# Kernel tuning notes

Hardware: AMD Instinct MI355X
Metric: run time of the kernel (lower is better)

The kernel has to match this reference:

```python
import jax, jax.numpy as jnp
import numpy as np

EMBED_DIM = 1024
NUM_HEADS = 16
HEAD_DIM = EMBED_DIM // NUM_HEADS
ROPE_BASE = 10000.0


def rotate_half(x):
    d = x.shape[-1] // 2
    x1, x2 = x[..., :d], x[..., d:]
    return jnp.concatenate((-x2, x1), axis=-1)


def setup_inputs() -> dict:
    key = jax.random.key(0)
    k_x, k_wqkv, k_bqkv, k_wo, k_bo = jax.random.split(key, 5)
    C = EMBED_DIM
    x = jax.random.normal(k_x, (4, 2048, C), dtype=jnp.float32)
    s = 1.0 / np.sqrt(C)
    W_qkv = jax.random.uniform(k_wqkv, (C, 3 * C), minval=-s, maxval=s, dtype=jnp.float32)
    b_qkv = jax.random.uniform(k_bqkv, (3 * C,), minval=-s, maxval=s, dtype=jnp.float32)
    W_out = jax.random.uniform(k_wo, (C, C), minval=-s, maxval=s, dtype=jnp.float32)
    b_out = jax.random.uniform(k_bo, (C,), minval=-s, maxval=s, dtype=jnp.float32)
    return {"x": x, "W_qkv": W_qkv, "b_qkv": b_qkv, "W_out": W_out, "b_out": b_out}


def reference(x, W_qkv, b_qkv, W_out, b_out):
    B, T, C = x.shape
    H, Dh = NUM_HEADS, HEAD_DIM
    # fused QKV projection: [B,T,3C] -> [3,B,H,T,Dh]
    qkv = (x @ W_qkv + b_qkv).reshape(B, T, 3, H, Dh).transpose(2, 0, 3, 1, 4)
    q, k, v = qkv[0], qkv[1], qkv[2]
    # rotary embedding: freqs [T, Dh/2] -> emb [T, Dh]
    inv_freq = 1.0 / (ROPE_BASE ** (jnp.arange(0, Dh, 2, dtype=jnp.float32) / Dh))
    freqs = jnp.arange(T, dtype=jnp.float32)[:, None] * inv_freq[None, :]
    emb = jnp.concatenate((freqs, freqs), axis=-1)  # [T, Dh], broadcasts over B,H
    cos, sin = jnp.cos(emb), jnp.sin(emb)
    q = q * cos + rotate_half(q) * sin
    k = k * cos + rotate_half(k) * sin
    # full (non-causal) attention, manual softmax
    scale = 1.0 / np.sqrt(Dh)
    attn = jax.nn.softmax(jnp.einsum("bhqd,bhkd->bhqk", q, k) * scale, axis=-1)
    out = jnp.einsum("bhqk,bhkd->bhqd", attn, v)  # [B,H,T,Dh]
    out = out.transpose(0, 2, 1, 3).reshape(B, T, C)
    return out @ W_out + b_out
```

## Files before the change

### kernel.cpp

```cpp
#include <hip/hip_runtime.h>
#include <math.h>

#define T_SEQ 2048
#define CDIM  1024
#define NH    16
#define DHD   64
#define BATCH 4
#define MROWS (BATCH * T_SEQ)
#define BHN   (BATCH * NH)

typedef _Float16 f16;
typedef __attribute__((ext_vector_type(8))) _Float16 f16x8;
typedef __attribute__((ext_vector_type(4))) _Float16 f16x4;
typedef __attribute__((ext_vector_type(2))) _Float16 f16x2;
typedef __attribute__((ext_vector_type(2))) __fp16 fp16x2;
typedef __attribute__((ext_vector_type(4))) float f32x4;

__device__ __forceinline__ float fast_exp2(float x) {
#if __has_builtin(__builtin_amdgcn_exp2f)
    return __builtin_amdgcn_exp2f(x);
#else
    return exp2f(x);
#endif
}

__device__ __forceinline__ float fast_rcp(float x) {
#if __has_builtin(__builtin_amdgcn_rcpf)
    return __builtin_amdgcn_rcpf(x);
#else
    return 1.0f / x;
#endif
}

__device__ __forceinline__ f16x2 cvt_pk_f16(float a, float b) {
    fp16x2 r = __builtin_amdgcn_cvt_pkrtz(a, b);
    return __builtin_bit_cast(f16x2, r);
}

__device__ __forceinline__ void gl_lds16(const f16* g, f16* l) {
    __builtin_amdgcn_global_load_lds(
        (const __attribute__((address_space(1))) void*)(g),
        (__attribute__((address_space(3))) void*)(l),
        16, 0, 0);
}

__global__ __launch_bounds__(256) void prep_kernel(
    const float* __restrict__ X, f16* __restrict__ Xf,
    const float* __restrict__ Wq, const float* __restrict__ Wo,
    f16* __restrict__ Wqt, f16* __restrict__ Wot,
    float* __restrict__ ctab, float* __restrict__ stab)
{
    const int bx = blockIdx.x;
    if (bx < 256) {
        int idx = bx * 256 + threadIdx.x;
        int t = idx >> 5, i = idx & 31;
        double inv = pow(10000.0, -(double)(2 * i) / 64.0);
        double a = (double)t * inv;
        ctab[idx] = (float)cos(a);
        stab[idx] = (float)sin(a);
    } else if (bx < 4352) {
        int idx = (bx - 256) * 256 + threadIdx.x;
        const float4* src = (const float4*)X + (size_t)idx * 2;
        float4 a = src[0], b = src[1];
        f16x8 o;
        o[0] = (f16)a.x; o[1] = (f16)a.y; o[2] = (f16)a.z; o[3] = (f16)a.w;
        o[4] = (f16)b.x; o[5] = (f16)b.y; o[6] = (f16)b.z; o[7] = (f16)b.w;
        *((f16x8*)Xf + idx) = o;
    } else {
        const int sub = threadIdx.x >> 6, lane = threadIdx.x & 63;
        const int id = (bx - 4352) * 4 + sub;
        const int k0 = (id & 127) * 8;
        const int ny = id >> 7;
        const float* W;
        f16* Wt;
        int N, n;
        if (ny < 48) { W = Wq; Wt = Wqt; N = 3072; n = ny * 64 + lane; }
        else         { W = Wo; Wt = Wot; N = 1024; n = (ny - 48) * 64 + lane; }
        f16x8 o;
#pragma unroll
        for (int j = 0; j < 8; j++) o[j] = (f16)W[(size_t)(k0 + j) * N + n];
        *(f16x8*)(Wt + (size_t)n * CDIM + k0) = o;
    }
}

#define GEMM_MAINLOOP(Aimg, Bimg, M0, N0)                                         \
    __shared__ f16 As[128][64], Bs[128][64];                                      \
    const int tid = threadIdx.x, wave = tid >> 6, lane = tid & 63;                \
    const int l16 = lane & 15, quad = lane >> 4;                                  \
    const int wm = wave >> 1, wn = wave & 1;                                      \
    f32x4 acc[4][4];                                                              \
    _Pragma("unroll") for (int i = 0; i < 4; i++)                                 \
        _Pragma("unroll") for (int j = 0; j < 4; j++)                             \
            acc[i][j] = (f32x4){0.f, 0.f, 0.f, 0.f};                              \
    const f16* sbase = (wave < 2) ? (Aimg) : (Bimg);                              \
    f16* lbase = ((wave < 2) ? &As[0][0] : &Bs[0][0]) + (wave & 1) * 4096;        \
    const size_t srow0 = ((wave < 2) ? (size_t)(M0) : (size_t)(N0)) + (wave & 1) * 64; \
    const int srow = lane >> 3, schunk = lane & 7;                                \
    const int gchunk = (schunk ^ srow) << 3;         \
    for (int k0 = 0; k0 < CDIM; k0 += 64) {                                       \
        _Pragma("unroll") for (int it = 0; it < 8; it++)                          \
            gl_lds16(sbase + (srow0 + it * 8 + srow) * CDIM + k0 + gchunk,        \
                     lbase + it * 512);                                           \
        __syncthreads();                                                          \
        _Pragma("unroll") for (int ks = 0; ks < 2; ks++) {                        \
            f16x8 fa[4], fb[4];                                                   \
            _Pragma("unroll") for (int mi = 0; mi < 4; mi++)                      \
                fa[mi] = *(const f16x8*)                                          \
                    &As[wm * 64 + mi * 16 + l16][((ks * 4 + quad) ^ (l16 & 7)) << 3]; \
            _Pragma("unroll") for (int ni = 0; ni < 4; ni++)                      \
                fb[ni] = *(const f16x8*)                                          \
                    &Bs[wn * 64 + ni * 16 + l16][((ks * 4 + quad) ^ (l16 & 7)) << 3]; \
            _Pragma("unroll") for (int mi = 0; mi < 4; mi++)                      \
                _Pragma("unroll") for (int ni = 0; ni < 4; ni++)                  \
                    acc[mi][ni] = __builtin_amdgcn_mfma_f32_16x16x32_f16(         \
                        fa[mi], fb[ni], acc[mi][ni], 0, 0, 0);                    \
        }                                                                         \
        __syncthreads();                                                          \
    }

__global__ __launch_bounds__(256) void qkv_gemm_kernel(
    const f16* __restrict__ Xf, const f16* __restrict__ Wt,
    const float* __restrict__ bias,
    const float* __restrict__ ctab, const float* __restrict__ stab,
    f16* __restrict__ qf, f16* __restrict__ kf, f16* __restrict__ vtb)
{
    const int m0 = blockIdx.x * 128;
    const int n0 = blockIdx.y * 128;
    GEMM_MAINLOOP(Xf, Wt, m0, n0)

    const int ncol0 = n0 + wn * 64;
    const int w = ncol0 >> 10;
    const int h = (ncol0 >> 6) & 15;
    const int b = m0 >> 11;
    const int trow0 = (m0 & 2047) + wm * 64 + quad * 4;
    float bia[4];
#pragma unroll
    for (int ni = 0; ni < 4; ni++) bia[ni] = bias[ncol0 + ni * 16 + l16];

    if (w < 2) {
        f16* oq = w ? kf : qf;
        const float sc = w ? 1.0f : 0.18033688011112042f;
#pragma unroll
        for (int mi = 0; mi < 4; mi++) {
#pragma unroll
            for (int i = 0; i < 4; i++) {
                int t = trow0 + mi * 16 + i;
                size_t rowoff = ((size_t)(b * NH + h) * T_SEQ + t) * DHD;
#pragma unroll
                for (int np = 0; np < 2; np++) {
                    int d = np * 16 + l16;
                    float v0 = acc[mi][np][i] + bia[np];
                    float v1 = acc[mi][np + 2][i] + bia[np + 2];
                    float c = ctab[(t << 5) + d];
                    float s = stab[(t << 5) + d];
                    oq[rowoff + d]      = (f16)((v0 * c - v1 * s) * sc);
                    oq[rowoff + d + 32] = (f16)((v1 * c + v0 * s) * sc);
                }
            }
        }
    } else {
#pragma unroll
        for (int mi = 0; mi < 4; mi++) {
            const int tb = trow0 + mi * 16;
#pragma unroll
            for (int ni = 0; ni < 4; ni++) {
                const int d = ni * 16 + l16;
                f16x4 pv;
#pragma unroll
                for (int i = 0; i < 4; i++) pv[i] = (f16)(acc[mi][ni][i] + bia[ni]);
                *(f16x4*)(vtb + ((size_t)(b * NH + h) * DHD + d) * T_SEQ + tb) = pv;
            }
        }
    }
}

__global__ __launch_bounds__(256, 4) void attn_kernel(
    const f16* __restrict__ qf, const f16* __restrict__ kf,
    const f16* __restrict__ vt, f16* __restrict__ ab)
{
    __shared__ f16 Kb[2][64][64];
    __shared__ f16 Vb[2][64][64];

    const int tid  = threadIdx.x;
    const int wave = tid >> 6, lane = tid & 63;
    const int l16  = lane & 15, quad = lane >> 4;

    const int flat = blockIdx.x + (blockIdx.y << 4);
    const int swz  = (flat & 7) * 128 + (flat >> 3);
    const int qt = swz & 15;
    const int bh = swz >> 4;
    const int q0 = qt * 128 + wave * 32;

    const f16* kbase = kf + (size_t)bh * T_SEQ * DHD;
    const f16* vbase = vt + (size_t)bh * DHD * T_SEQ;

    f16x8 qfr[2][2];
#pragma unroll
    for (int qs = 0; qs < 2; qs++) {
        const f16* qrow = qf + ((size_t)bh * T_SEQ + q0 + qs * 16 + l16) * DHD;
        qfr[qs][0] = *(const f16x8*)(qrow + quad * 8);
        qfr[qs][1] = *(const f16x8*)(qrow + 32 + quad * 8);
    }

    f32x4 o[2][4];
    f32x4 lacc[2];
#pragma unroll
    for (int qs = 0; qs < 2; qs++) {
        lacc[qs] = (f32x4){0.f, 0.f, 0.f, 0.f};
#pragma unroll
        for (int dt = 0; dt < 4; dt++) o[qs][dt] = (f32x4){0.f, 0.f, 0.f, 0.f};
    }
    f16x4 ones4;
#pragma unroll
    for (int j = 0; j < 4; j++) ones4[j] = (f16)1.0f;

    const int srow = tid >> 3;
    const int schunk = tid & 7;
    const int gcol = (schunk ^ (srow & 7)) << 3;

#define STAGE(t, b)                                                               \
    {                                                                             \
        const f16* kg = kbase + ((size_t)(t) * 64 + srow) * DHD + gcol;           \
        const f16* vg = vbase + (size_t)srow * T_SEQ + (t) * 64 + gcol;           \
        f16* kl = &Kb[b][wave * 8][0];                                            \
        f16* vl = &Vb[b][wave * 8][0];                                            \
        gl_lds16(kg, kl);                                                         \
        gl_lds16(kg + 32 * DHD, kl + 32 * 64);                                    \
        gl_lds16(vg, vl);                                                         \
        gl_lds16(vg + (size_t)32 * T_SEQ, vl + 32 * 64);                          \
    }

    STAGE(0, 0)
    __syncthreads();

    for (int kt = 0; kt < 32; kt++) {
        const int buf = kt & 1;
        if (kt < 31) STAGE(kt + 1, buf ^ 1)

#pragma unroll
        for (int half = 0; half < 2; half++) {
            f32x4 sc[2][2];
#pragma unroll
            for (int k2 = 0; k2 < 2; k2++)
#pragma unroll
                for (int qs = 0; qs < 2; qs++) sc[k2][qs] = (f32x4){0.f, 0.f, 0.f, 0.f};
            __builtin_amdgcn_s_setprio(1);
#pragma unroll
            for (int k2 = 0; k2 < 2; k2++) {
                const int keyt = half * 2 + k2;
#pragma unroll
                for (int ks = 0; ks < 2; ks++) {
                    const int kc = ((ks * 4 + quad) ^ (l16 & 7)) << 3;
                    f16x8 kfr = *(const f16x8*)&Kb[buf][keyt * 16 + l16][kc];
#pragma unroll
                    for (int qs = 0; qs < 2; qs++)
                        sc[k2][qs] = __builtin_amdgcn_mfma_f32_16x16x32_f16(
                            kfr, qfr[qs][ks], sc[k2][qs], 0, 0, 0);
                }
            }
            __builtin_amdgcn_s_setprio(0);
            f16x4 pp[2][2];
#pragma unroll
            for (int k2 = 0; k2 < 2; k2++) {
#pragma unroll
                for (int qs = 0; qs < 2; qs++) {
                    ((f16x2*)&pp[k2][qs])[0] = cvt_pk_f16(
                        fast_exp2(sc[k2][qs][0]), fast_exp2(sc[k2][qs][1]));
                    ((f16x2*)&pp[k2][qs])[1] = cvt_pk_f16(
                        fast_exp2(sc[k2][qs][2]), fast_exp2(sc[k2][qs][3]));
                }
            }
            __builtin_amdgcn_s_setprio(1);
#pragma unroll
            for (int qs = 0; qs < 2; qs++)
#pragma unroll
                for (int k2 = 0; k2 < 2; k2++)
                    lacc[qs] = __builtin_amdgcn_mfma_f32_16x16x16f16(
                        pp[k2][qs], ones4, lacc[qs], 0, 0, 0);
#pragma unroll
            for (int dt = 0; dt < 4; dt++) {
#pragma unroll
                for (int c = 0; c < 2; c++) {
                    const int vc = ((half * 4 + c * 2 + (quad >> 1)) ^ (l16 & 7)) * 8
                                 + (quad & 1) * 4;
                    f16x4 vfr = *(const f16x4*)&Vb[buf][dt * 16 + l16][vc];
#pragma unroll
                    for (int qs = 0; qs < 2; qs++)
                        o[qs][dt] = __builtin_amdgcn_mfma_f32_16x16x16f16(
                            pp[c][qs], vfr, o[qs][dt], 0, 0, 0);
                }
            }
            __builtin_amdgcn_s_setprio(0);
        }

        if (kt < 31) __syncthreads();
    }
#undef STAGE

    const int b = bh >> 4, h = bh & 15;
#pragma unroll
    for (int qs = 0; qs < 2; qs++) {
#pragma unroll
        for (int i = 0; i < 4; i++) {
            float iv = fast_rcp(lacc[qs][i]);
            int m = b * T_SEQ + qt * 128 + wave * 32 + qs * 16 + quad * 4 + i;
#pragma unroll
            for (int dt = 0; dt < 4; dt++)
                ab[(size_t)m * CDIM + h * 64 + dt * 16 + l16] = (f16)(o[qs][dt][i] * iv);
        }
    }
}

__global__ __launch_bounds__(256) void out_gemm_kernel(
    const f16* __restrict__ Ab, const f16* __restrict__ Wt,
    const float* __restrict__ bias, float* __restrict__ out)
{
    const int m0 = blockIdx.x * 128;
    const int n0 = blockIdx.y * 128;
    GEMM_MAINLOOP(Ab, Wt, m0, n0)

    const int ncol0 = n0 + wn * 64;
    float bia[4];
#pragma unroll
    for (int ni = 0; ni < 4; ni++) bia[ni] = bias[ncol0 + ni * 16 + l16];
#pragma unroll
    for (int mi = 0; mi < 4; mi++) {
#pragma unroll
        for (int i = 0; i < 4; i++) {
            int m = m0 + wm * 64 + mi * 16 + quad * 4 + i;
#pragma unroll
            for (int ni = 0; ni < 4; ni++)
                out[(size_t)m * CDIM + ncol0 + ni * 16 + l16] = acc[mi][ni][i] + bia[ni];
        }
    }
}

extern "C" void kernel_launch(void* const* d_in, const int* in_sizes, int n_in,
                              void* d_out, int out_size, void* d_ws, size_t ws_size,
                              hipStream_t stream)
{
    const float* x    = (const float*)d_in[0];
    const float* Wqkv = (const float*)d_in[1];
    const float* bqkv = (const float*)d_in[2];
    const float* Wout = (const float*)d_in[3];
    const float* bout = (const float*)d_in[4];
    float* out = (float*)d_out;

    const size_t XSZ  = (size_t)MROWS * CDIM;
    const size_t WQSZ = (size_t)3072 * CDIM;
    const size_t WOSZ = (size_t)CDIM * CDIM;
    const size_t QSZ  = (size_t)BHN * T_SEQ * DHD;

    char* p = (char*)d_ws;
    f16* Xf  = (f16*)p; p += XSZ * 2;
    f16* Wqt = (f16*)p; p += WQSZ * 2;
    f16* Wot = (f16*)p; p += WOSZ * 2;
    f16* qf  = (f16*)p; p += QSZ * 2;
    f16* kf  = (f16*)p; p += QSZ * 2;
    f16* vtb = (f16*)p; p += QSZ * 2;
    f16* ab  = (f16*)p; p += QSZ * 2;
    float* ctab = (float*)p; p += T_SEQ * 32 * 4;
    float* stab = (float*)p; p += T_SEQ * 32 * 4;

    prep_kernel<<<6400, 256, 0, stream>>>(x, Xf, Wqkv, Wout, Wqt, Wot, ctab, stab);
    qkv_gemm_kernel<<<dim3(64, 24), 256, 0, stream>>>(
        Xf, Wqt, bqkv, ctab, stab, qf, kf, vtb);
    attn_kernel<<<dim3(16, BHN), 256, 0, stream>>>(qf, kf, vtb, ab);
    out_gemm_kernel<<<dim3(64, 8), 256, 0, stream>>>(ab, Wot, bout, out);
}
```

Baseline: 276.4 us.

## Switch attention to 32x32x16 MFMA tiles with permlane-swapped P operands

Rewrites the attention inner loop to use 32x32x16 f16 MFMAs for both QK^T and PV instead of 16x16 tiles. The exp'd probabilities are repacked into the A-operand layout with v_permlane32_swap, so no LDS round trip is needed. The row sum is now accumulated on the VALU and reduced through a cross-half shuffle plus a small LDS buffer, replacing the ones-vector MFMA. The aim is fewer MFMA issues and fewer LDS reads per tile, at the cost of larger accumulator register pressure and an extra barrier at the end.

```diff
diff --git a/kernel.cpp b/kernel.cpp
--- a/kernel.cpp
+++ b/kernel.cpp
@@ -15,6 +15,8 @@
 typedef __attribute__((ext_vector_type(2))) _Float16 f16x2;
 typedef __attribute__((ext_vector_type(2))) __fp16 fp16x2;
 typedef __attribute__((ext_vector_type(4))) float f32x4;
+typedef __attribute__((ext_vector_type(16))) float f32x16;
+typedef __attribute__((ext_vector_type(4))) unsigned int uint4v;
 
 __device__ __forceinline__ float fast_exp2(float x) {
 #if __has_builtin(__builtin_amdgcn_exp2f)
@@ -35,6 +37,10 @@
 __device__ __forceinline__ f16x2 cvt_pk_f16(float a, float b) {
     fp16x2 r = __builtin_amdgcn_cvt_pkrtz(a, b);
     return __builtin_bit_cast(f16x2, r);
+}
+
+__device__ __forceinline__ void permlane32_swap(unsigned &a, unsigned &b) {
+    asm volatile("v_permlane32_swap_b32 %0, %1" : "+v"(a), "+v"(b));
 }
 
 __device__ __forceinline__ void gl_lds16(const f16* g, f16* l) {
@@ -180,10 +186,11 @@
 {
     __shared__ f16 Kb[2][64][64];
     __shared__ f16 Vb[2][64][64];
+    __shared__ float Lb[4][32];
 
     const int tid  = threadIdx.x;
     const int wave = tid >> 6, lane = tid & 63;
-    const int l16  = lane & 15, quad = lane >> 4;
+    const int l31  = lane & 31, hh = lane >> 5;
 
     const int flat = blockIdx.x + (blockIdx.y << 4);
     const int swz  = (flat & 7) * 128 + (flat >> 3);
@@ -194,25 +201,20 @@
     const f16* kbase = kf + (size_t)bh * T_SEQ * DHD;
     const f16* vbase = vt + (size_t)bh * DHD * T_SEQ;
 
-    f16x8 qfr[2][2];
-#pragma unroll
-    for (int qs = 0; qs < 2; qs++) {
-        const f16* qrow = qf + ((size_t)bh * T_SEQ + q0 + qs * 16 + l16) * DHD;
-        qfr[qs][0] = *(const f16x8*)(qrow + quad * 8);
-        qfr[qs][1] = *(const f16x8*)(qrow + 32 + quad * 8);
-    }
-
-    f32x4 o[2][4];
-    f32x4 lacc[2];
-#pragma unroll
-    for (int qs = 0; qs < 2; qs++) {
-        lacc[qs] = (f32x4){0.f, 0.f, 0.f, 0.f};
-#pragma unroll
-        for (int dt = 0; dt < 4; dt++) o[qs][dt] = (f32x4){0.f, 0.f, 0.f, 0.f};
-    }
-    f16x4 ones4;
-#pragma unroll
-    for (int j = 0; j < 4; j++) ones4[j] = (f16)1.0f;
+    f16x8 qfr[4];
+    {
+        const f16* qrow = qf + ((size_t)bh * T_SEQ + q0 + l31) * DHD + hh * 8;
+#pragma unroll
+        for (int kk = 0; kk < 4; kk++)
+            qfr[kk] = *(const f16x8*)(qrow + kk * 16);
+    }
+
+    f32x16 o[2];
+#pragma unroll
+    for (int db = 0; db < 2; db++)
+#pragma unroll
+        for (int r = 0; r < 16; r++) o[db][r] = 0.f;
+    float lacc = 0.f;
 
     const int srow = tid >> 3;
     const int schunk = tid & 7;
@@ -237,77 +239,75 @@
         const int buf = kt & 1;
         if (kt < 31) STAGE(kt + 1, buf ^ 1)
 
-#pragma unroll
-        for (int half = 0; half < 2; half++) {
-            f32x4 sc[2][2];
-#pragma unroll
-            for (int k2 = 0; k2 < 2; k2++)
-#pragma unroll
-                for (int qs = 0; qs < 2; qs++) sc[k2][qs] = (f32x4){0.f, 0.f, 0.f, 0.f};
+        f16x8 pA[4];
+#pragma unroll
+        for (int b2 = 0; b2 < 2; b2++) {
+            f32x16 scc;
+#pragma unroll
+            for (int r = 0; r < 16; r++) scc[r] = 0.f;
             __builtin_amdgcn_s_setprio(1);
 #pragma unroll
-            for (int k2 = 0; k2 < 2; k2++) {
-                const int keyt = half * 2 + k2;
-#pragma unroll
-                for (int ks = 0; ks < 2; ks++) {
-                    const int kc = ((ks * 4 + quad) ^ (l16 & 7)) << 3;
-                    f16x8 kfr = *(const f16x8*)&Kb[buf][keyt * 16 + l16][kc];
-#pragma unroll
-                    for (int qs = 0; qs < 2; qs++)
-                        sc[k2][qs] = __builtin_amdgcn_mfma_f32_16x16x32_f16(
-                            kfr, qfr[qs][ks], sc[k2][qs], 0, 0, 0);
-                }
+            for (int kk = 0; kk < 4; kk++) {
+                const int kc = ((kk * 2 + hh) ^ (l31 & 7)) << 3;
+                f16x8 kfr = *(const f16x8*)&Kb[buf][b2 * 32 + l31][kc];
+                scc = __builtin_amdgcn_mfma_f32_32x32x16_f16(
+                    kfr, qfr[kk], scc, 0, 0, 0);
             }
             __builtin_amdgcn_s_setprio(0);
-            f16x4 pp[2][2];
-#pragma unroll
-            for (int k2 = 0; k2 < 2; k2++) {
-#pragma unroll
-                for (int qs = 0; qs < 2; qs++) {
-                    ((f16x2*)&pp[k2][qs])[0] = cvt_pk_f16(
-                        fast_exp2(sc[k2][qs][0]), fast_exp2(sc[k2][qs][1]));
-                    ((f16x2*)&pp[k2][qs])[1] = cvt_pk_f16(
-                        fast_exp2(sc[k2][qs][2]), fast_exp2(sc[k2][qs][3]));
-                }
-            }
-            __builtin_amdgcn_s_setprio(1);
-#pragma unroll
-            for (int qs = 0; qs < 2; qs++)
-#pragma unroll
-                for (int k2 = 0; k2 < 2; k2++)
-                    lacc[qs] = __builtin_amdgcn_mfma_f32_16x16x16f16(
-                        pp[k2][qs], ones4, lacc[qs], 0, 0, 0);
-#pragma unroll
-            for (int dt = 0; dt < 4; dt++) {
-#pragma unroll
-                for (int c = 0; c < 2; c++) {
-                    const int vc = ((half * 4 + c * 2 + (quad >> 1)) ^ (l16 & 7)) * 8
-                                 + (quad & 1) * 4;
-                    f16x4 vfr = *(const f16x4*)&Vb[buf][dt * 16 + l16][vc];
-#pragma unroll
-                    for (int qs = 0; qs < 2; qs++)
-                        o[qs][dt] = __builtin_amdgcn_mfma_f32_16x16x16f16(
-                            pp[c][qs], vfr, o[qs][dt], 0, 0, 0);
-                }
-            }
-            __builtin_amdgcn_s_setprio(0);
-        }
+            float e[16];
+#pragma unroll
+            for (int r = 0; r < 16; r++) {
+                e[r] = fast_exp2(scc[r]);
+                lacc += e[r];
+            }
+            unsigned pk[8];
+#pragma unroll
+            for (int i = 0; i < 8; i++)
+                pk[i] = __builtin_bit_cast(unsigned,
+                                           cvt_pk_f16(e[2 * i], e[2 * i + 1]));
+            permlane32_swap(pk[0], pk[2]);
+            permlane32_swap(pk[1], pk[3]);
+            permlane32_swap(pk[4], pk[6]);
+            permlane32_swap(pk[5], pk[7]);
+            uint4v a0 = {pk[0], pk[1], pk[2], pk[3]};
+            uint4v a1 = {pk[4], pk[5], pk[6], pk[7]};
+            pA[b2 * 2]     = __builtin_bit_cast(f16x8, a0);
+            pA[b2 * 2 + 1] = __builtin_bit_cast(f16x8, a1);
+        }
+        __builtin_amdgcn_s_setprio(1);
+#pragma unroll
+        for (int db = 0; db < 2; db++) {
+#pragma unroll
+            for (int kk = 0; kk < 4; kk++) {
+                const int vc = ((kk * 2 + hh) ^ (l31 & 7)) << 3;
+                f16x8 vfr = *(const f16x8*)&Vb[buf][db * 32 + l31][vc];
+                o[db] = __builtin_amdgcn_mfma_f32_32x32x16_f16(
+                    pA[kk], vfr, o[db], 0, 0, 0);
+            }
+        }
+        __builtin_amdgcn_s_setprio(0);
 
         if (kt < 31) __syncthreads();
     }
 #undef STAGE
 
+    lacc += __shfl_xor(lacc, 32);
+    if (lane < 32) Lb[wave][l31] = lacc;
+    __syncthreads();
+    f32x4 ivv[4];
+#pragma unroll
+    for (int g = 0; g < 4; g++)
+        ivv[g] = *(const f32x4*)&Lb[wave][g * 8 + hh * 4];
+
     const int b = bh >> 4, h = bh & 15;
 #pragma unroll
-    for (int qs = 0; qs < 2; qs++) {
-#pragma unroll
-        for (int i = 0; i < 4; i++) {
-            float iv = fast_rcp(lacc[qs][i]);
-            int m = b * T_SEQ + qt * 128 + wave * 32 + qs * 16 + quad * 4 + i;
-#pragma unroll
-            for (int dt = 0; dt < 4; dt++)
-                ab[(size_t)m * CDIM + h * 64 + dt * 16 + l16] = (f16)(o[qs][dt][i] * iv);
-        }
+    for (int r = 0; r < 16; r++) {
+        const int qrow = (r & 3) + 8 * (r >> 2) + 4 * hh;
+        const int m = b * T_SEQ + qt * 128 + wave * 32 + qrow;
+        const float iv = fast_rcp(ivv[r >> 2][r & 3]);
+        f16* dst = ab + (size_t)m * CDIM + h * 64 + l31;
+        dst[0]  = (f16)(o[0][r] * iv);
+        dst[32] = (f16)(o[1][r] * iv);
     }
 }
 
```

Measured after the change: 276.7 us. No clear change (+0.1%).
